# Kernel tuning notes

Hardware: AMD Instinct MI355X
Metric: run time of the kernel (lower is better)

## Reference

```python
import jax, jax.numpy as jnp
import numpy as np

N, DEG, C, D = 4096, 12, 4, 2
E = N * DEG
P = 2 * (D + 1) ** 2          # 18 radial MLPs: value set (s=0) + attention-key set (s=1)
R_MAX = (2 * D + 1) * C * C   # largest radial output size = 80


def _ln(x, g, b, eps=1e-5):
    mu = jnp.mean(x, axis=-1, keepdims=True)
    var = jnp.mean((x - mu) ** 2, axis=-1, keepdims=True)
    return (x - mu) / jnp.sqrt(var + eps) * g + b


def setup_inputs() -> dict:
    key = jax.random.key(0)
    ks = jax.random.split(key, 40)
    inp = {}
    inp["u"] = jax.random.randint(ks[0], (E,), 0, N)   # src nodes
    inp["v"] = jnp.repeat(jnp.arange(N), DEG)           # dst nodes: every node has DEG in-edges
    inp["dist"] = jax.random.uniform(ks[1], (E,))
    for k in range(D + 1):
        inp[f"f{k}"] = jax.random.normal(ks[2 + k], (N, C, 2 * k + 1))
    i = 5
    for k in range(D + 1):
        for l in range(D + 1):
            J = 2 * min(k, l) + 1
            inp[f"wj_{k}{l}"] = jax.random.normal(ks[i], (E, J, 2 * l + 1, 2 * k + 1)) * 0.2
            i += 1
    inp["wq"] = jax.random.normal(ks[i], (D + 1, C, C)) * 0.4; i += 1
    inp["rad_W1"] = jax.random.normal(ks[i], (P, 16, C + 1)) * 0.3; i += 1
    inp["rad_b1"] = jnp.zeros((P, 16)); inp["rad_g1"] = jnp.ones((P, 16)); inp["rad_be1"] = jnp.zeros((P, 16))
    inp["rad_W2"] = jax.random.normal(ks[i], (P, 16, 16)) * 0.25; i += 1
    inp["rad_b2"] = jnp.zeros((P, 16)); inp["rad_g2"] = jnp.ones((P, 16)); inp["rad_be2"] = jnp.zeros((P, 16))
    inp["rad_W3"] = jax.random.normal(ks[i], (P, R_MAX, 16)) * 0.2; i += 1
    inp["rad_b3"] = jnp.zeros((P, R_MAX))
    inp["si_W1"] = jax.random.normal(ks[i], (D + 1, C * C, C * C)) * 0.25; i += 1
    inp["si_b1"] = jnp.zeros((D + 1, C * C)); inp["si_g1"] = jnp.ones((D + 1, C * C)); inp["si_be1"] = jnp.zeros((D + 1, C * C))
    inp["si_W2"] = jax.random.normal(ks[i], (D + 1, C * C, C * C)) * 0.25; i += 1
    inp["si_b2"] = jnp.zeros((D + 1, C * C)); inp["si_g2"] = jnp.ones((D + 1, C * C)); inp["si_be2"] = jnp.zeros((D + 1, C * C))
    inp["si_W3"] = jax.random.normal(ks[i], (D + 1, C * C, C * C)) * 0.25; i += 1
    inp["si_b3"] = jnp.zeros((D + 1, C * C))
    return inp


def _forward(u, v, dist, f0, f1, f2,
             wj_00, wj_01, wj_02, wj_10, wj_11, wj_12, wj_20, wj_21, wj_22,
             wq, rad_W1, rad_b1, rad_g1, rad_be1, rad_W2, rad_b2, rad_g2, rad_be2, rad_W3, rad_b3,
             si_W1, si_b1, si_g1, si_be1, si_W2, si_b2, si_g2, si_be2, si_W3, si_b3):
    f = [f0, f1, f2]
    wj = {(0, 0): wj_00, (0, 1): wj_01, (0, 2): wj_02,
          (1, 0): wj_10, (1, 1): wj_11, (1, 2): wj_12,
          (2, 0): wj_20, (2, 1): wj_21, (2, 2): wj_22}
    n = f0.shape[0]
    # shared radial input: per-channel <f0_u, f0_v> plus edge distance -> [E, C+1]
    iv = jnp.concatenate([jnp.sum(f0[u] * f0[v], axis=2), dist[:, None]], axis=1)

    def radial(p, J):
        r_size = J * C * C
        h = jax.nn.relu(_ln(iv @ rad_W1[p].T + rad_b1[p], rad_g1[p], rad_be1[p]))
        h = jax.nn.relu(_ln(h @ rad_W2[p].T + rad_b2[p], rad_g2[p], rad_be2[p]))
        return h @ rad_W3[p, :r_size].T + rad_b3[p, :r_size]

    def make_w(k, l, s):
        # WLayer: radial MLP -> [E, J, c_out, c_in], contracted with CG basis w_j
        J = 2 * min(k, l) + 1
        p = s * (D + 1) ** 2 + k * (D + 1) + l
        Rm = radial(p, J).reshape(-1, J, C, C)
        return jnp.einsum('ejoi,ejlk->eoilk', Rm, wj[(k, l)])  # [E,o,i,2l+1,2k+1]

    # --- attention (AttnBlock) ---
    q = jnp.concatenate([jnp.einsum('oi,nik->nok', wq[k], f[k]) for k in range(D + 1)], axis=2)  # [N,C,9]
    k_edge = jnp.concatenate([
        sum(jnp.einsum('eoilk,eik->eol', make_w(k, l, 1), f[k][v]) for k in range(D + 1))
        for l in range(D + 1)], axis=2)  # [E,C,9] (keys use dst features, as in calc_k)
    dot = jnp.einsum('eol,eol->e', q[v], k_edge)
    m = jax.ops.segment_max(dot, v, num_segments=n)
    lse = m + jnp.log(jax.ops.segment_sum(jnp.exp(dot - m[v]), v, num_segments=n))
    a = jnp.exp(dot - lse[v])  # edge softmax over incoming edges of each dst node

    # --- attention-weighted tensor-product messages + scatter-sum (update_all) ---
    outs = []
    for l in range(D + 1):
        vl = sum(jnp.einsum('e,eoilk,eik->eol', a, make_w(k, l, 0), f[k][u]) for k in range(D + 1))
        outs.append(jax.ops.segment_sum(vl, v, num_segments=n))  # [N,C,2l+1]

    # --- self-interaction ---
    for l in range(D + 1):
        inner = jnp.einsum('ncl,ndl->ncd', f[l], f[l]).reshape(n, C * C)
        h = jax.nn.relu(_ln(inner @ si_W1[l].T + si_b1[l], si_g1[l], si_be1[l]))
        h = jax.nn.relu(_ln(h @ si_W2[l].T + si_b2[l], si_g2[l], si_be2[l]))
        siw = (h @ si_W3[l].T + si_b3[l]).reshape(n, C, C)
        outs[l] = outs[l] + jnp.einsum('noi,nil->nol', siw, f[l])

    # concat degree outputs f_out[0..2] along the m-axis -> [N, C, 1+3+5]
    return jnp.concatenate(outs, axis=2)


def reference(u, v, dist, f0, f1, f2,
              wj_00, wj_01, wj_02, wj_10, wj_11, wj_12, wj_20, wj_21, wj_22,
              wq, rad_W1, rad_b1, rad_g1, rad_be1, rad_W2, rad_b2, rad_g2, rad_be2, rad_W3, rad_b3,
              si_W1, si_b1, si_g1, si_be1, si_W2, si_b2, si_g2, si_be2, si_W3, si_b3):
    return _forward(u, v, dist, f0, f1, f2,
                    wj_00, wj_01, wj_02, wj_10, wj_11, wj_12, wj_20, wj_21, wj_22,
                    wq, rad_W1, rad_b1, rad_g1, rad_be1, rad_W2, rad_b2, rad_g2, rad_be2, rad_W3, rad_b3,
                    si_W1, si_b1, si_g1, si_be1, si_W2, si_b2, si_g2, si_be2, si_W3, si_b3)
```

## Files before the change

kernel.cpp:

```cpp
#include <hip/hip_runtime.h>
#include <hip/hip_bf16.h>

#define DEG 12

struct GP {
  const int* u;
  const void* dist;
  const void* f0; const void* f1; const void* f2;
  const void* wj[9];
  const void* wq;
  const void *rW1,*rb1,*rg1,*rbe1,*rW2,*rb2,*rg2,*rbe2,*rW3,*rb3;
  const void *sW1,*sb1,*sg1,*sbe1,*sW2,*sb2,*sg2,*sbe2,*sW3,*sb3;
  void* out;
  const float* wsf;
};

#define WS_W1   0
#define WS_W2   1440
#define WS_W3   6048
#define WS_SI1  29088
#define WS_SI2  29856
#define WS_SI3  30624
#define WS_G1   31392
#define WS_BE1  31680
#define WS_G2   31968
#define WS_BE2  32256
#define WS_B1   32544
#define WS_B2   32832
#define WS_B3   33120
#define WS_TOTAL 34560

struct alignas(16) Smem {
  float sRm[DEG][308];
  float sG[DEG][276];
  float sH2[DEG][148];
  float sF[13][36];
  float sIv[DEG][5];
  float sQ[36];
  float sDot[DEG];
  float sA[DEG];
  float sVl[DEG][36];
  float sSIin[48], sSIh[48], sSIh2[48], sSiw[48];
};

__device__ __forceinline__ float ldv(const __hip_bfloat16* p, int i){ return __bfloat162float(p[i]); }
__device__ __forceinline__ float ldv(const float* p, int i){ return p[i]; }

__device__ __forceinline__ void load16(const __hip_bfloat16* ptr, float* out){
  const uint4* q = reinterpret_cast<const uint4*>(ptr);
  uint4 a = q[0]; uint4 b = q[1];
  unsigned w[8] = {a.x,a.y,a.z,a.w,b.x,b.y,b.z,b.w};
  #pragma unroll
  for (int i=0;i<8;i++){
    out[2*i]   = __uint_as_float(w[i] << 16);
    out[2*i+1] = __uint_as_float(w[i] & 0xffff0000u);
  }
}
__device__ __forceinline__ void load16(const float* ptr, float* out){
  const float4* q = reinterpret_cast<const float4*>(ptr);
  #pragma unroll
  for (int i=0;i<4;i++){
    float4 a = q[i];
    out[4*i]=a.x; out[4*i+1]=a.y; out[4*i+2]=a.z; out[4*i+3]=a.w;
  }
}

__device__ __forceinline__ void st(__hip_bfloat16* p, int i, float v){ p[i] = __float2bfloat16(v); }
__device__ __forceinline__ void st(float* p, int i, float v){ p[i] = v; }

template<typename WT>
__device__ __forceinline__ void ln_relu16(float* h, const WT* g, const WT* be){
  float mu = 0.f;
  #pragma unroll
  for (int c=0;c<16;c++) mu += h[c];
  mu *= 0.0625f;
  float var = 0.f;
  #pragma unroll
  for (int c=0;c<16;c++){ float d=h[c]-mu; var += d*d; }
  var *= 0.0625f;
  float inv = rsqrtf(var + 1e-5f);
  #pragma unroll
  for (int c=0;c<16;c++){
    float y = (h[c]-mu)*inv*ldv(g,c) + ldv(be,c);
    h[c] = fmaxf(y, 0.f);
  }
}

template<typename WT>
struct WPtr {
  const WT *w1,*w2,*w3,*si1,*si2,*si3,*g1,*be1,*g2,*be2,*b1,*b2,*b3;
};

template<typename WT>
__device__ __forceinline__ void radial12(int S, const WPtr<WT>& W, int t, Smem& s){
  const int pk = t/12, e = t%12;
  const int pp = S*9 + pk;
  const float x0=s.sIv[e][0],x1=s.sIv[e][1],x2=s.sIv[e][2],x3=s.sIv[e][3],x4=s.sIv[e][4];
  float h[16];
  #pragma unroll
  for (int r=0;r<16;r++){
    const WT* row = W.w1 + (pp*16+r)*5;
    h[r] = ldv(W.b1,pp*16+r) + ldv(row,0)*x0 + ldv(row,1)*x1
         + ldv(row,2)*x2 + ldv(row,3)*x3 + ldv(row,4)*x4;
  }
  ln_relu16(h, W.g1+pp*16, W.be1+pp*16);
  float h2[16];
  #pragma unroll
  for (int r=0;r<16;r++){
    float wf[16]; load16(W.w2 + (pp*16+r)*16, wf);
    float acc = ldv(W.b2,pp*16+r);
    #pragma unroll
    for (int c=0;c<16;c++) acc += wf[c]*h[c];
    h2[r]=acc;
  }
  ln_relu16(h2, W.g2+pp*16, W.be2+pp*16);
  float4* dst = (float4*)&s.sH2[e][pk*16];
  #pragma unroll
  for (int i=0;i<4;i++) dst[i] = make_float4(h2[4*i],h2[4*i+1],h2[4*i+2],h2[4*i+3]);
}

template<typename WT>
__device__ __forceinline__ void radial3(int S, const WPtr<WT>& W, int t, Smem& s){
  const int rq = t/3, eq = t%3;
  const int rflat = rq*4;
  constexpr int RS[10]={0,16,32,48,64,112,160,176,224,304};
  int kp=0;
  #pragma unroll
  for (int k=1;k<9;k++) if (rflat >= RS[k]) kp = k;
  const int rl = rflat - RS[kp];
  const int pp = S*9 + kp;
  const int wbase = (pp*80 + rl)*16;
  float b[4];
  #pragma unroll
  for (int r=0;r<4;r++) b[r] = ldv(W.b3, pp*80+rl+r);
  #pragma unroll
  for (int half=0; half<2; ++half){
    const int e0 = eq*4 + half*2, e1 = e0+1;
    const float4* hp0 = (const float4*)&s.sH2[e0][kp*16];
    const float4* hp1 = (const float4*)&s.sH2[e1][kp*16];
    float4 ha[4], hb[4];
    #pragma unroll
    for (int i=0;i<4;i++){ ha[i]=hp0[i]; hb[i]=hp1[i]; }
    float a0[4], a1[4];
    #pragma unroll
    for (int r=0;r<4;r++){
      float wf[16]; load16(W.w3 + wbase + r*16, wf);
      float s0=0.f, s1=0.f;
      const float* h0 = (const float*)&ha[0];
      const float* h1 = (const float*)&hb[0];
      #pragma unroll
      for (int c=0;c<16;c++){ s0 += wf[c]*h0[c]; s1 += wf[c]*h1[c]; }
      a0[r]=b[r]+s0; a1[r]=b[r]+s1;
    }
    *(float4*)&s.sRm[e0][rflat] = make_float4(a0[0],a0[1],a0[2],a0[3]);
    *(float4*)&s.sRm[e1][rflat] = make_float4(a1[0],a1[1],a1[2],a1[3]);
  }
}

template<typename T>
__device__ __forceinline__ void stage_g(int S, const GP& p, int tt, int n12, Smem& s){
  constexpr int GOFF[9]={0,4,16,36,40,76,136,140,176};
  #pragma unroll
  for (int kp=0;kp<9;kp++){
    const int kk=kp/3, ll=kp%3;
    const int mn = kk<ll?kk:ll;
    const int J=2*mn+1, Lm=2*ll+1, Km=2*kk+1;
    const int koff = (kk==0)?0:((kk==1)?4:16);
    const int goff = GOFF[kp];
    const T* wjp = (const T*)p.wj[kp];
    const int nt = 12*J*Lm;
    for (int q=tt; q<nt; q+=128){
      int e = q/(J*Lm), jl = q%(J*Lm);
      int j = jl/Lm, lm = jl%Lm;
      const T* w = wjp + ((size_t)((n12+e)*J + j)*Lm + lm)*Km;
      const float* fv = S ? &s.sF[12][koff] : &s.sF[e][koff];
      float a0=0.f,a1=0.f,a2=0.f,a3=0.f;
      #pragma unroll
      for (int km=0;km<Km;km++){
        float wv = ldv(w,km);
        a0 += wv*fv[0*Km+km];
        a1 += wv*fv[1*Km+km];
        a2 += wv*fv[2*Km+km];
        a3 += wv*fv[3*Km+km];
      }
      float* gd = &s.sG[e][goff];
      gd[(j*4+0)*Lm+lm]=a0;
      gd[(j*4+1)*Lm+lm]=a1;
      gd[(j*4+2)*Lm+lm]=a2;
      gd[(j*4+3)*Lm+lm]=a3;
    }
  }
}

template<typename T, typename WT>
__device__ void gconv_run(const GP& p, Smem& s, const WPtr<WT>& W){
  const int n = blockIdx.x;
  const int t = threadIdx.x;
  const int n12 = n*DEG;
  const T* f0=(const T*)p.f0; const T* f1=(const T*)p.f1; const T* f2=(const T*)p.f2;
  constexpr int ROFF[9]={0,16,32,48,64,112,160,176,224};
  constexpr int GOFF[9]={0,4,16,36,40,76,136,140,176};

  for (int q0=t; q0<13*36; q0+=256){
    int node=q0/36, j=q0%36;
    int idn = (node<DEG)? p.u[n12+node] : n;
    float v;
    if (j<4)       v = ldv(f0, idn*4  + j);
    else if (j<16) v = ldv(f1, idn*12 + (j-4));
    else           v = ldv(f2, idn*20 + (j-16));
    s.sF[node][j] = v;
  }
  __syncthreads();

  if (t<48){ int e=t>>2, c=t&3; s.sIv[e][c] = s.sF[e][c]*s.sF[12][c]; }
  else if (t<60){ int e=t-48; s.sIv[e][4] = ldv((const T*)p.dist, n12+e); }
  else if (t>=64 && t<100){
    int t2=t-64, o=t2/9, mc=t2%9;
    int k = (mc<1)?0:((mc<4)?1:2);
    int m = mc - ((k==0)?0:((k==1)?1:4));
    int koff=(k==0)?0:((k==1)?4:16), Km=2*k+1;
    float acc=0.f;
    #pragma unroll
    for (int i=0;i<4;i++) acc += ldv((const T*)p.wq,(k*4+o)*4+i) * s.sF[12][koff+i*Km+m];
    s.sQ[t2]=acc;
  } else if (t>=128 && t<176){
    int t3=t-128, l=t3/16, rr=t3%16, o=rr>>2, i=rr&3;
    int koff=(l==0)?0:((l==1)?4:16), Lm=2*l+1;
    float acc=0.f;
    for (int m=0;m<Lm;m++) acc += s.sF[12][koff+o*Lm+m]*s.sF[12][koff+i*Lm+m];
    s.sSIin[t3]=acc;
  }
  __syncthreads();

  if (t<108)       radial12(1, W, t, s);
  else if (t>=128) stage_g<T>(1, p, t-128, n12, s);
  __syncthreads();

  if (t<228) radial3(1, W, t, s);
  __syncthreads();

  if (t<192){
    const int e=t>>4, o=(t>>2)&3, i=t&3;
    float d=0.f;
    #pragma unroll
    for (int kp=0;kp<9;kp++){
      const int kk=kp/3, ll=kp%3;
      const int mn=kk<ll?kk:ll;
      const int J=2*mn+1, Lm=2*ll+1;
      const int loff=(ll==0)?0:((ll==1)?1:4);
      #pragma unroll
      for (int j=0;j<J;j++){
        float rm = s.sRm[e][ROFF[kp]+j*16+o*4+i];
        #pragma unroll
        for (int lm=0;lm<Lm;lm++)
          d += rm * s.sG[e][GOFF[kp]+(j*4+i)*Lm+lm] * s.sQ[o*9+loff+lm];
      }
    }
    d += __shfl_xor(d,1);
    d += __shfl_xor(d,2);
    d += __shfl_xor(d,4);
    d += __shfl_xor(d,8);
    if ((t&15)==0) s.sDot[e]=d;
  } else if (t<240){
    int idx=t-192, l=idx/16, r=idx%16;
    float wf[16]; load16(W.si1 + (l*16+r)*16, wf);
    float acc = ldv((const T*)p.sb1,l*16+r);
    #pragma unroll
    for (int c=0;c<16;c++) acc += wf[c]*s.sSIin[l*16+c];
    s.sSIh[idx]=acc;
  }
  __syncthreads();

  if (t<108)       radial12(0, W, t, s);
  else if (t==127){
    float mx=-1e30f;
    #pragma unroll
    for (int e=0;e<12;e++) mx = fmaxf(mx, s.sDot[e]);
    float ex[12]; float se=0.f;
    #pragma unroll
    for (int e=0;e<12;e++){ ex[e]=__expf(s.sDot[e]-mx); se += ex[e]; }
    #pragma unroll
    for (int e=0;e<12;e++) s.sA[e] = ex[e]/se;
  }
  else if (t>=128) stage_g<T>(0, p, t-128, n12, s);
  __syncthreads();

  if (t<228) radial3(0, W, t, s);
  __syncthreads();

  if (t>=64){
    for (int q=t-64; q<432; q+=192){
      int l,e,o,lm;
      if (q<48){ l=0; e=q>>2; o=q&3; lm=0; }
      else if (q<192){ int r=q-48; l=1; e=r/12; int r2=r%12; o=r2/3; lm=r2%3; }
      else { int r=q-192; l=2; e=r/20; int r2=r%20; o=r2/5; lm=r2%5; }
      const int Lm=2*l+1, loff=(l==0)?0:((l==1)?1:4);
      float acc=0.f;
      for (int kk=0;kk<3;kk++){
        const int kp=kk*3+l;
        const int mn=kk<l?kk:l;
        const int J=2*mn+1;
        for (int j=0;j<J;j++)
          #pragma unroll
          for (int i=0;i<4;i++)
            acc += s.sRm[e][ROFF[kp]+j*16+o*4+i] * s.sG[e][GOFF[kp]+(j*4+i)*Lm+lm];
      }
      s.sVl[e][o*9+loff+lm]=acc;
    }
  } else if (t<48){
    int l=t/16, r=t%16;
    float mu=0.f;
    #pragma unroll
    for (int c=0;c<16;c++) mu += s.sSIh[l*16+c];
    mu *= 0.0625f;
    float var=0.f;
    #pragma unroll
    for (int c=0;c<16;c++){ float d=s.sSIh[l*16+c]-mu; var+=d*d; }
    var *= 0.0625f;
    float inv = rsqrtf(var+1e-5f);
    float wf[16]; load16(W.si2 + (l*16+r)*16, wf);
    float acc = ldv((const T*)p.sb2,l*16+r);
    #pragma unroll
    for (int c=0;c<16;c++){
      float y = (s.sSIh[l*16+c]-mu)*inv*ldv((const T*)p.sg1,l*16+c) + ldv((const T*)p.sbe1,l*16+c);
      acc += wf[c]*fmaxf(y,0.f);
    }
    s.sSIh2[t]=acc;
  }
  __syncthreads();

  if (t<48){
    int l=t/16, r=t%16;
    float mu=0.f;
    #pragma unroll
    for (int c=0;c<16;c++) mu += s.sSIh2[l*16+c];
    mu *= 0.0625f;
    float var=0.f;
    #pragma unroll
    for (int c=0;c<16;c++){ float d=s.sSIh2[l*16+c]-mu; var+=d*d; }
    var *= 0.0625f;
    float inv = rsqrtf(var+1e-5f);
    float wf[16]; load16(W.si3 + (l*16+r)*16, wf);
    float acc = ldv((const T*)p.sb3,l*16+r);
    #pragma unroll
    for (int c=0;c<16;c++){
      float y = (s.sSIh2[l*16+c]-mu)*inv*ldv((const T*)p.sg2,l*16+c) + ldv((const T*)p.sbe2,l*16+c);
      acc += wf[c]*fmaxf(y,0.f);
    }
    s.sSiw[t]=acc;
  }
  __syncthreads();

  if (t<36){
    int o=t/9, mc=t%9;
    int l = (mc<1)?0:((mc<4)?1:2);
    int m = mc - ((l==0)?0:((l==1)?1:4));
    int koff=(l==0)?0:((l==1)?4:16), Lm=2*l+1;
    float acc=0.f;
    #pragma unroll
    for (int e=0;e<12;e++) acc += s.sA[e]*s.sVl[e][t];
    #pragma unroll
    for (int i=0;i<4;i++) acc += s.sSiw[l*16+o*4+i]*s.sF[12][koff+i*Lm+m];
    st((T*)p.out, n*36+t, acc);
  }
}

template<typename T>
__device__ __forceinline__ void gconv_dispatch(const GP& p, Smem& s){
  if (p.wsf){
    const float* w = p.wsf;
    WPtr<float> W{w+WS_W1, w+WS_W2, w+WS_W3, w+WS_SI1, w+WS_SI2, w+WS_SI3,
                  w+WS_G1, w+WS_BE1, w+WS_G2, w+WS_BE2, w+WS_B1, w+WS_B2, w+WS_B3};
    gconv_run<T,float>(p, s, W);
  } else {
    WPtr<T> W{(const T*)p.rW1,(const T*)p.rW2,(const T*)p.rW3,
              (const T*)p.sW1,(const T*)p.sW2,(const T*)p.sW3,
              (const T*)p.rg1,(const T*)p.rbe1,(const T*)p.rg2,(const T*)p.rbe2,
              (const T*)p.rb1,(const T*)p.rb2,(const T*)p.rb3};
    gconv_run<T,T>(p, s, W);
  }
}

__global__ __launch_bounds__(256,4) void gconv_kernel(GP p){
  __shared__ Smem s;
  const unsigned magic = *(const unsigned*)p.rg1;
  if (magic == 0x3F803F80u) gconv_dispatch<__hip_bfloat16>(p, s);
  else                      gconv_dispatch<float>(p, s);
}

template<typename T>
__device__ __forceinline__ void prep_body(const GP& p, float* ws, int i){
  float v;
  if      (i<WS_W2)  v = ldv((const T*)p.rW1,  i-WS_W1);
  else if (i<WS_W3)  v = ldv((const T*)p.rW2,  i-WS_W2);
  else if (i<WS_SI1) v = ldv((const T*)p.rW3,  i-WS_W3);
  else if (i<WS_SI2) v = ldv((const T*)p.sW1,  i-WS_SI1);
  else if (i<WS_SI3) v = ldv((const T*)p.sW2,  i-WS_SI2);
  else if (i<WS_G1)  v = ldv((const T*)p.sW3,  i-WS_SI3);
  else if (i<WS_BE1) v = ldv((const T*)p.rg1,  i-WS_G1);
  else if (i<WS_G2)  v = ldv((const T*)p.rbe1, i-WS_BE1);
  else if (i<WS_BE2) v = ldv((const T*)p.rg2,  i-WS_G2);
  else if (i<WS_B1)  v = ldv((const T*)p.rbe2, i-WS_BE2);
  else if (i<WS_B2)  v = ldv((const T*)p.rb1,  i-WS_B1);
  else if (i<WS_B3)  v = ldv((const T*)p.rb2,  i-WS_B2);
  else               v = ldv((const T*)p.rb3,  i-WS_B3);
  ws[i] = v;
}

__global__ void prep_kernel(GP p, float* ws){
  int i = blockIdx.x*256 + threadIdx.x;
  if (i >= WS_TOTAL) return;
  const unsigned magic = *(const unsigned*)p.rg1;
  if (magic == 0x3F803F80u) prep_body<__hip_bfloat16>(p, ws, i);
  else                      prep_body<float>(p, ws, i);
}

extern "C" void kernel_launch(void* const* d_in, const int* in_sizes, int n_in,
                              void* d_out, int out_size, void* d_ws, size_t ws_size,
                              hipStream_t stream) {
  GP p;
  p.u    = (const int*)d_in[0];
  p.dist = d_in[2];
  p.f0   = d_in[3];
  p.f1   = d_in[4];
  p.f2   = d_in[5];
  for (int kp=0;kp<9;kp++) p.wj[kp] = d_in[6+kp];
  p.wq   = d_in[15];
  p.rW1  = d_in[16]; p.rb1  = d_in[17]; p.rg1  = d_in[18]; p.rbe1 = d_in[19];
  p.rW2  = d_in[20]; p.rb2  = d_in[21]; p.rg2  = d_in[22]; p.rbe2 = d_in[23];
  p.rW3  = d_in[24]; p.rb3  = d_in[25];
  p.sW1  = d_in[26]; p.sb1  = d_in[27]; p.sg1  = d_in[28]; p.sbe1 = d_in[29];
  p.sW2  = d_in[30]; p.sb2  = d_in[31]; p.sg2  = d_in[32]; p.sbe2 = d_in[33];
  p.sW3  = d_in[34]; p.sb3  = d_in[35];
  p.out  = d_out;

  const bool use_ws = (ws_size >= (size_t)WS_TOTAL*sizeof(float));
  p.wsf = use_ws ? (const float*)d_ws : nullptr;

  if (use_ws)
    prep_kernel<<<dim3((WS_TOTAL+255)/256), dim3(256), 0, stream>>>(p, (float*)d_ws);
  gconv_kernel<<<dim3(4096), dim3(256), 0, stream>>>(p);
}
```

Baseline: 269.7 us.

## Fold radial output contraction into radial3 and drop sRm shared buffer

The last radial layer now contracts its outputs directly with the staged G tensor, accumulating attention dot products and value vectors into shared memory with atomics. This removes the 12x308 sRm buffer and two separate contraction phases with their barriers. The self-interaction MLP steps are moved onto otherwise idle threads of earlier phases. Launch bounds rise to 6 blocks per SM to take advantage of the smaller shared footprint. The cost is shared-memory atomic contention and register pressure under the tighter bound.

```diff
diff --git a/kernel.cpp b/kernel.cpp
--- a/kernel.cpp
+++ b/kernel.cpp
@@ -31,15 +31,14 @@
 #define WS_TOTAL 34560
 
 struct alignas(16) Smem {
-  float sRm[DEG][308];
   float sG[DEG][276];
   float sH2[DEG][148];
   float sF[13][36];
+  float sVl[DEG][36];
   float sIv[DEG][5];
   float sQ[36];
   float sDot[DEG];
   float sA[DEG];
-  float sVl[DEG][36];
   float sSIin[48], sSIh[48], sSIh2[48], sSiw[48];
 };
 
@@ -119,26 +118,33 @@
   for (int i=0;i<4;i++) dst[i] = make_float4(h2[4*i],h2[4*i+1],h2[4*i+2],h2[4*i+3]);
 }
 
-template<typename WT>
-__device__ __forceinline__ void radial3(int S, const WPtr<WT>& W, int t, Smem& s){
+template<int S, typename WT>
+__device__ __forceinline__ void radial3fold(const WPtr<WT>& W, int t, Smem& s){
+  constexpr int GOFF[9]={0,4,16,36,40,76,136,140,176};
+  constexpr int RS[10]={0,16,32,48,64,112,160,176,224,304};
   const int rq = t/3, eq = t%3;
   const int rflat = rq*4;
-  constexpr int RS[10]={0,16,32,48,64,112,160,176,224,304};
   int kp=0;
   #pragma unroll
   for (int k=1;k<9;k++) if (rflat >= RS[k]) kp = k;
   const int rl = rflat - RS[kp];
+  const int j = rl>>4, o=(rl>>2)&3;
   const int pp = S*9 + kp;
   const int wbase = (pp*80 + rl)*16;
+  const int ll = kp%3;
+  const int Lm = 2*ll+1;
+  const int loff = (ll==0)?0:((ll==1)?1:4);
+  const int goff = GOFF[kp] + (j*4)*Lm;
   float b[4];
   #pragma unroll
   for (int r=0;r<4;r++) b[r] = ldv(W.b3, pp*80+rl+r);
+
   #pragma unroll
   for (int half=0; half<2; ++half){
     const int e0 = eq*4 + half*2, e1 = e0+1;
+    float4 ha[4], hb[4];
     const float4* hp0 = (const float4*)&s.sH2[e0][kp*16];
     const float4* hp1 = (const float4*)&s.sH2[e1][kp*16];
-    float4 ha[4], hb[4];
     #pragma unroll
     for (int i=0;i<4;i++){ ha[i]=hp0[i]; hb[i]=hp1[i]; }
     float a0[4], a1[4];
@@ -146,14 +152,31 @@
     for (int r=0;r<4;r++){
       float wf[16]; load16(W.w3 + wbase + r*16, wf);
       float s0=0.f, s1=0.f;
-      const float* h0 = (const float*)&ha[0];
-      const float* h1 = (const float*)&hb[0];
+      const float* h0=(const float*)ha; const float* h1=(const float*)hb;
       #pragma unroll
       for (int c=0;c<16;c++){ s0 += wf[c]*h0[c]; s1 += wf[c]*h1[c]; }
       a0[r]=b[r]+s0; a1[r]=b[r]+s1;
     }
-    *(float4*)&s.sRm[e0][rflat] = make_float4(a0[0],a0[1],a0[2],a0[3]);
-    *(float4*)&s.sRm[e1][rflat] = make_float4(a1[0],a1[1],a1[2],a1[3]);
+    const float* g0 = &s.sG[e0][goff];
+    const float* g1 = &s.sG[e1][goff];
+    if (S==1){
+      float d0=0.f, d1=0.f;
+      for (int lm=0; lm<Lm; lm++){
+        float q = s.sQ[o*9+loff+lm];
+        float u0 = a0[0]*g0[lm] + a0[1]*g0[Lm+lm] + a0[2]*g0[2*Lm+lm] + a0[3]*g0[3*Lm+lm];
+        float u1 = a1[0]*g1[lm] + a1[1]*g1[Lm+lm] + a1[2]*g1[2*Lm+lm] + a1[3]*g1[3*Lm+lm];
+        d0 += q*u0; d1 += q*u1;
+      }
+      atomicAdd(&s.sDot[e0], d0);
+      atomicAdd(&s.sDot[e1], d1);
+    } else {
+      for (int lm=0; lm<Lm; lm++){
+        float u0 = a0[0]*g0[lm] + a0[1]*g0[Lm+lm] + a0[2]*g0[2*Lm+lm] + a0[3]*g0[3*Lm+lm];
+        float u1 = a1[0]*g1[lm] + a1[1]*g1[Lm+lm] + a1[2]*g1[2*Lm+lm] + a1[3]*g1[3*Lm+lm];
+        atomicAdd(&s.sVl[e0][o*9+loff+lm], u0);
+        atomicAdd(&s.sVl[e1][o*9+loff+lm], u1);
+      }
+    }
   }
 }
 
@@ -198,8 +221,6 @@
   const int t = threadIdx.x;
   const int n12 = n*DEG;
   const T* f0=(const T*)p.f0; const T* f1=(const T*)p.f1; const T* f2=(const T*)p.f2;
-  constexpr int ROFF[9]={0,16,32,48,64,112,160,176,224};
-  constexpr int GOFF[9]={0,4,16,36,40,76,136,140,176};
 
   for (int q0=t; q0<13*36; q0+=256){
     int node=q0/36, j=q0%36;
@@ -210,6 +231,11 @@
     else           v = ldv(f2, idn*20 + (j-16));
     s.sF[node][j] = v;
   }
+  {
+    float* z = &s.sVl[0][0];
+    for (int q=t; q<432; q+=256) z[q]=0.f;
+    if (t<12) s.sDot[t]=0.f;
+  }
   __syncthreads();
 
   if (t<48){ int e=t>>2, c=t&3; s.sIv[e][c] = s.sF[e][c]*s.sF[12][c]; }
@@ -232,46 +258,25 @@
   }
   __syncthreads();
 
-  if (t<108)       radial12(1, W, t, s);
-  else if (t>=128) stage_g<T>(1, p, t-128, n12, s);
-  __syncthreads();
-
-  if (t<228) radial3(1, W, t, s);
-  __syncthreads();
-
-  if (t<192){
-    const int e=t>>4, o=(t>>2)&3, i=t&3;
-    float d=0.f;
-    #pragma unroll
-    for (int kp=0;kp<9;kp++){
-      const int kk=kp/3, ll=kp%3;
-      const int mn=kk<ll?kk:ll;
-      const int J=2*mn+1, Lm=2*ll+1;
-      const int loff=(ll==0)?0:((ll==1)?1:4);
-      #pragma unroll
-      for (int j=0;j<J;j++){
-        float rm = s.sRm[e][ROFF[kp]+j*16+o*4+i];
-        #pragma unroll
-        for (int lm=0;lm<Lm;lm++)
-          d += rm * s.sG[e][GOFF[kp]+(j*4+i)*Lm+lm] * s.sQ[o*9+loff+lm];
-      }
-    }
-    d += __shfl_xor(d,1);
-    d += __shfl_xor(d,2);
-    d += __shfl_xor(d,4);
-    d += __shfl_xor(d,8);
-    if ((t&15)==0) s.sDot[e]=d;
-  } else if (t<240){
-    int idx=t-192, l=idx/16, r=idx%16;
-    float wf[16]; load16(W.si1 + (l*16+r)*16, wf);
-    float acc = ldv((const T*)p.sb1,l*16+r);
-    #pragma unroll
-    for (int c=0;c<16;c++) acc += wf[c]*s.sSIin[l*16+c];
-    s.sSIh[idx]=acc;
-  }
-  __syncthreads();
-
-  if (t<108)       radial12(0, W, t, s);
+  if (t<108) radial12(1, W, t, s);
+  else if (t>=128){
+    stage_g<T>(1, p, t-128, n12, s);
+    const int tt=t-128;
+    if (tt<48){
+      int l=tt/16, r=tt%16;
+      float wf[16]; load16(W.si1 + (l*16+r)*16, wf);
+      float acc = ldv((const T*)p.sb1,l*16+r);
+      #pragma unroll
+      for (int c=0;c<16;c++) acc += wf[c]*s.sSIin[l*16+c];
+      s.sSIh[tt]=acc;
+    }
+  }
+  __syncthreads();
+
+  if (t<228) radial3fold<1>(W, t, s);
+  __syncthreads();
+
+  if (t<108) radial12(0, W, t, s);
   else if (t==127){
     float mx=-1e30f;
     #pragma unroll
@@ -282,72 +287,54 @@
     #pragma unroll
     for (int e=0;e<12;e++) s.sA[e] = ex[e]/se;
   }
-  else if (t>=128) stage_g<T>(0, p, t-128, n12, s);
-  __syncthreads();
-
-  if (t<228) radial3(0, W, t, s);
-  __syncthreads();
-
-  if (t>=64){
-    for (int q=t-64; q<432; q+=192){
-      int l,e,o,lm;
-      if (q<48){ l=0; e=q>>2; o=q&3; lm=0; }
-      else if (q<192){ int r=q-48; l=1; e=r/12; int r2=r%12; o=r2/3; lm=r2%3; }
-      else { int r=q-192; l=2; e=r/20; int r2=r%20; o=r2/5; lm=r2%5; }
-      const int Lm=2*l+1, loff=(l==0)?0:((l==1)?1:4);
-      float acc=0.f;
-      for (int kk=0;kk<3;kk++){
-        const int kp=kk*3+l;
-        const int mn=kk<l?kk:l;
-        const int J=2*mn+1;
-        for (int j=0;j<J;j++)
-          #pragma unroll
-          for (int i=0;i<4;i++)
-            acc += s.sRm[e][ROFF[kp]+j*16+o*4+i] * s.sG[e][GOFF[kp]+(j*4+i)*Lm+lm];
+  else if (t>=128){
+    stage_g<T>(0, p, t-128, n12, s);
+    const int tt=t-128;
+    if (tt<48){
+      int l=tt/16, r=tt%16;
+      float mu=0.f;
+      #pragma unroll
+      for (int c=0;c<16;c++) mu += s.sSIh[l*16+c];
+      mu *= 0.0625f;
+      float var=0.f;
+      #pragma unroll
+      for (int c=0;c<16;c++){ float d=s.sSIh[l*16+c]-mu; var+=d*d; }
+      var *= 0.0625f;
+      float inv = rsqrtf(var+1e-5f);
+      float wf[16]; load16(W.si2 + (l*16+r)*16, wf);
+      float acc = ldv((const T*)p.sb2,l*16+r);
+      #pragma unroll
+      for (int c=0;c<16;c++){
+        float y = (s.sSIh[l*16+c]-mu)*inv*ldv((const T*)p.sg1,l*16+c) + ldv((const T*)p.sbe1,l*16+c);
+        acc += wf[c]*fmaxf(y,0.f);
       }
-      s.sVl[e][o*9+loff+lm]=acc;
-    }
-  } else if (t<48){
-    int l=t/16, r=t%16;
-    float mu=0.f;
-    #pragma unroll
-    for (int c=0;c<16;c++) mu += s.sSIh[l*16+c];
-    mu *= 0.0625f;
-    float var=0.f;
-    #pragma unroll
-    for (int c=0;c<16;c++){ float d=s.sSIh[l*16+c]-mu; var+=d*d; }
-    var *= 0.0625f;
-    float inv = rsqrtf(var+1e-5f);
-    float wf[16]; load16(W.si2 + (l*16+r)*16, wf);
-    float acc = ldv((const T*)p.sb2,l*16+r);
-    #pragma unroll
-    for (int c=0;c<16;c++){
-      float y = (s.sSIh[l*16+c]-mu)*inv*ldv((const T*)p.sg1,l*16+c) + ldv((const T*)p.sbe1,l*16+c);
-      acc += wf[c]*fmaxf(y,0.f);
-    }
-    s.sSIh2[t]=acc;
-  }
-  __syncthreads();
-
-  if (t<48){
-    int l=t/16, r=t%16;
-    float mu=0.f;
-    #pragma unroll
-    for (int c=0;c<16;c++) mu += s.sSIh2[l*16+c];
-    mu *= 0.0625f;
-    float var=0.f;
-    #pragma unroll
-    for (int c=0;c<16;c++){ float d=s.sSIh2[l*16+c]-mu; var+=d*d; }
-    var *= 0.0625f;
-    float inv = rsqrtf(var+1e-5f);
-    float wf[16]; load16(W.si3 + (l*16+r)*16, wf);
-    float acc = ldv((const T*)p.sb3,l*16+r);
-    #pragma unroll
-    for (int c=0;c<16;c++){
-      float y = (s.sSIh2[l*16+c]-mu)*inv*ldv((const T*)p.sg2,l*16+c) + ldv((const T*)p.sbe2,l*16+c);
-      acc += wf[c]*fmaxf(y,0.f);
-    }
-    s.sSiw[t]=acc;
+      s.sSIh2[tt]=acc;
+    }
+  }
+  __syncthreads();
+
+  if (t<228) radial3fold<0>(W, t, s);
+  else {
+    for (int q=t-228; q<48; q+=28){
+      int l=q/16, r=q%16;
+      float mu=0.f;
+      #pragma unroll
+      for (int c=0;c<16;c++) mu += s.sSIh2[l*16+c];
+      mu *= 0.0625f;
+      float var=0.f;
+      #pragma unroll
+      for (int c=0;c<16;c++){ float d=s.sSIh2[l*16+c]-mu; var+=d*d; }
+      var *= 0.0625f;
+      float inv = rsqrtf(var+1e-5f);
+      float wf[16]; load16(W.si3 + (l*16+r)*16, wf);
+      float acc = ldv((const T*)p.sb3,l*16+r);
+      #pragma unroll
+      for (int c=0;c<16;c++){
+        float y = (s.sSIh2[l*16+c]-mu)*inv*ldv((const T*)p.sg2,l*16+c) + ldv((const T*)p.sbe2,l*16+c);
+        acc += wf[c]*fmaxf(y,0.f);
+      }
+      s.sSiw[q]=acc;
+    }
   }
   __syncthreads();
 
@@ -381,7 +368,7 @@
   }
 }
 
-__global__ __launch_bounds__(256,4) void gconv_kernel(GP p){
+__global__ __launch_bounds__(256,6) void gconv_kernel(GP p){
   __shared__ Smem s;
   const unsigned magic = *(const unsigned*)p.rg1;
   if (magic == 0x3F803F80u) gconv_dispatch<__hip_bfloat16>(p, s);
```

After: 572.5 us. +112.2%, slower.

## Split radial MLP rows across thread pairs and rebalance per-stage thread work

Applied to the files above, without the earlier changes.

Each radial-MLP (pp,edge) unit is now handled by two threads, each computing 8 of the 16 hidden rows, with layer-norm statistics and activations exchanged via shuffles, so 216 threads work instead of 108. Stage assignments are reshuffled: the self-interaction MLP layers move into the idle lanes of the radial stages, stage_g for the value set runs on all 256 threads in its own phase, and the value contraction uses all threads. This aims to shorten the serial critical path of each block's barrier-separated phases, at the cost of extra shuffles and duplicate weight-row loads per pair, plus one added barrier phase.

```diff
diff --git a/kernel.cpp b/kernel.cpp
--- a/kernel.cpp
+++ b/kernel.cpp
@@ -69,54 +69,75 @@
 __device__ __forceinline__ void st(float* p, int i, float v){ p[i] = v; }
 
 template<typename WT>
-__device__ __forceinline__ void ln_relu16(float* h, const WT* g, const WT* be){
-  float mu = 0.f;
-  #pragma unroll
-  for (int c=0;c<16;c++) mu += h[c];
-  mu *= 0.0625f;
-  float var = 0.f;
-  #pragma unroll
-  for (int c=0;c<16;c++){ float d=h[c]-mu; var += d*d; }
-  var *= 0.0625f;
-  float inv = rsqrtf(var + 1e-5f);
-  #pragma unroll
-  for (int c=0;c<16;c++){
-    float y = (h[c]-mu)*inv*ldv(g,c) + ldv(be,c);
-    h[c] = fmaxf(y, 0.f);
-  }
-}
-
-template<typename WT>
 struct WPtr {
   const WT *w1,*w2,*w3,*si1,*si2,*si3,*g1,*be1,*g2,*be2,*b1,*b2,*b3;
 };
 
 template<typename WT>
-__device__ __forceinline__ void radial12(int S, const WPtr<WT>& W, int t, Smem& s){
-  const int pk = t/12, e = t%12;
+__device__ __forceinline__ void radial12_split(int S, const WPtr<WT>& W, int t, Smem& s){
+  const int u = t>>1, b = t&1;
+  const int pk = u/12, e = u%12;
   const int pp = S*9 + pk;
+  const int rbase = pp*16 + b*8;
   const float x0=s.sIv[e][0],x1=s.sIv[e][1],x2=s.sIv[e][2],x3=s.sIv[e][3],x4=s.sIv[e][4];
-  float h[16];
-  #pragma unroll
-  for (int r=0;r<16;r++){
-    const WT* row = W.w1 + (pp*16+r)*5;
-    h[r] = ldv(W.b1,pp*16+r) + ldv(row,0)*x0 + ldv(row,1)*x1
+  float h[8];
+  #pragma unroll
+  for (int r=0;r<8;r++){
+    const WT* row = W.w1 + (rbase+r)*5;
+    h[r] = ldv(W.b1,rbase+r) + ldv(row,0)*x0 + ldv(row,1)*x1
          + ldv(row,2)*x2 + ldv(row,3)*x3 + ldv(row,4)*x4;
   }
-  ln_relu16(h, W.g1+pp*16, W.be1+pp*16);
-  float h2[16];
-  #pragma unroll
-  for (int r=0;r<16;r++){
-    float wf[16]; load16(W.w2 + (pp*16+r)*16, wf);
-    float acc = ldv(W.b2,pp*16+r);
-    #pragma unroll
-    for (int c=0;c<16;c++) acc += wf[c]*h[c];
+  float s1=0.f;
+  #pragma unroll
+  for (int c=0;c<8;c++) s1 += h[c];
+  s1 += __shfl_xor(s1,1);
+  const float mu = s1*0.0625f;
+  float v1=0.f;
+  #pragma unroll
+  for (int c=0;c<8;c++){ float d=h[c]-mu; v1 += d*d; }
+  v1 += __shfl_xor(v1,1);
+  const float inv = rsqrtf(v1*0.0625f + 1e-5f);
+  #pragma unroll
+  for (int c=0;c<8;c++){
+    float y = (h[c]-mu)*inv*ldv(W.g1,rbase+c) + ldv(W.be1,rbase+c);
+    h[c] = fmaxf(y,0.f);
+  }
+  float lo[8], hi[8];
+  #pragma unroll
+  for (int c=0;c<8;c++){
+    float o = __shfl_xor(h[c],1);
+    lo[c] = b ? o : h[c];
+    hi[c] = b ? h[c] : o;
+  }
+  float h2[8];
+  #pragma unroll
+  for (int r=0;r<8;r++){
+    float wf[16]; load16(W.w2 + (rbase+r)*16, wf);
+    float acc = ldv(W.b2,rbase+r);
+    #pragma unroll
+    for (int c=0;c<8;c++) acc += wf[c]*lo[c];
+    #pragma unroll
+    for (int c=0;c<8;c++) acc += wf[8+c]*hi[c];
     h2[r]=acc;
   }
-  ln_relu16(h2, W.g2+pp*16, W.be2+pp*16);
-  float4* dst = (float4*)&s.sH2[e][pk*16];
-  #pragma unroll
-  for (int i=0;i<4;i++) dst[i] = make_float4(h2[4*i],h2[4*i+1],h2[4*i+2],h2[4*i+3]);
+  float s2=0.f;
+  #pragma unroll
+  for (int c=0;c<8;c++) s2 += h2[c];
+  s2 += __shfl_xor(s2,1);
+  const float mu2 = s2*0.0625f;
+  float v2=0.f;
+  #pragma unroll
+  for (int c=0;c<8;c++){ float d=h2[c]-mu2; v2 += d*d; }
+  v2 += __shfl_xor(v2,1);
+  const float inv2 = rsqrtf(v2*0.0625f + 1e-5f);
+  #pragma unroll
+  for (int c=0;c<8;c++){
+    float y = (h2[c]-mu2)*inv2*ldv(W.g2,rbase+c) + ldv(W.be2,rbase+c);
+    h2[c] = fmaxf(y,0.f);
+  }
+  float4* dst = (float4*)&s.sH2[e][pk*16 + b*8];
+  dst[0] = make_float4(h2[0],h2[1],h2[2],h2[3]);
+  dst[1] = make_float4(h2[4],h2[5],h2[6],h2[7]);
 }
 
 template<typename WT>
@@ -158,7 +179,7 @@
 }
 
 template<typename T>
-__device__ __forceinline__ void stage_g(int S, const GP& p, int tt, int n12, Smem& s){
+__device__ __forceinline__ void stage_g(int S, const GP& p, int tt, int nthr, int n12, Smem& s){
   constexpr int GOFF[9]={0,4,16,36,40,76,136,140,176};
   #pragma unroll
   for (int kp=0;kp<9;kp++){
@@ -169,7 +190,7 @@
     const int goff = GOFF[kp];
     const T* wjp = (const T*)p.wj[kp];
     const int nt = 12*J*Lm;
-    for (int q=tt; q<nt; q+=128){
+    for (int q=tt; q<nt; q+=nthr){
       int e = q/(J*Lm), jl = q%(J*Lm);
       int j = jl/Lm, lm = jl%Lm;
       const T* w = wjp + ((size_t)((n12+e)*J + j)*Lm + lm)*Km;
@@ -223,17 +244,28 @@
     #pragma unroll
     for (int i=0;i<4;i++) acc += ldv((const T*)p.wq,(k*4+o)*4+i) * s.sF[12][koff+i*Km+m];
     s.sQ[t2]=acc;
-  } else if (t>=128 && t<176){
-    int t3=t-128, l=t3/16, rr=t3%16, o=rr>>2, i=rr&3;
+  } else if (t>=100 && t<148){
+    int t3=t-100, l=t3/16, rr=t3%16, o=rr>>2, i=rr&3;
     int koff=(l==0)?0:((l==1)?4:16), Lm=2*l+1;
     float acc=0.f;
     for (int m=0;m<Lm;m++) acc += s.sF[12][koff+o*Lm+m]*s.sF[12][koff+i*Lm+m];
     s.sSIin[t3]=acc;
-  }
-  __syncthreads();
-
-  if (t<108)       radial12(1, W, t, s);
-  else if (t>=128) stage_g<T>(1, p, t-128, n12, s);
+  } else if (t>=148){
+    stage_g<T>(1, p, t-148, 108, n12, s);
+  }
+  __syncthreads();
+
+  if (t<216) radial12_split(1, W, t, s);
+  else {
+    for (int q=t-216; q<48; q+=40){
+      int l=q/16, r=q%16;
+      float wf[16]; load16(W.si1 + (l*16+r)*16, wf);
+      float acc = ldv((const T*)p.sb1,l*16+r);
+      #pragma unroll
+      for (int c=0;c<16;c++) acc += wf[c]*s.sSIin[l*16+c];
+      s.sSIh[q]=acc;
+    }
+  }
   __syncthreads();
 
   if (t<228) radial3(1, W, t, s);
@@ -263,52 +295,6 @@
     if ((t&15)==0) s.sDot[e]=d;
   } else if (t<240){
     int idx=t-192, l=idx/16, r=idx%16;
-    float wf[16]; load16(W.si1 + (l*16+r)*16, wf);
-    float acc = ldv((const T*)p.sb1,l*16+r);
-    #pragma unroll
-    for (int c=0;c<16;c++) acc += wf[c]*s.sSIin[l*16+c];
-    s.sSIh[idx]=acc;
-  }
-  __syncthreads();
-
-  if (t<108)       radial12(0, W, t, s);
-  else if (t==127){
-    float mx=-1e30f;
-    #pragma unroll
-    for (int e=0;e<12;e++) mx = fmaxf(mx, s.sDot[e]);
-    float ex[12]; float se=0.f;
-    #pragma unroll
-    for (int e=0;e<12;e++){ ex[e]=__expf(s.sDot[e]-mx); se += ex[e]; }
-    #pragma unroll
-    for (int e=0;e<12;e++) s.sA[e] = ex[e]/se;
-  }
-  else if (t>=128) stage_g<T>(0, p, t-128, n12, s);
-  __syncthreads();
-
-  if (t<228) radial3(0, W, t, s);
-  __syncthreads();
-
-  if (t>=64){
-    for (int q=t-64; q<432; q+=192){
-      int l,e,o,lm;
-      if (q<48){ l=0; e=q>>2; o=q&3; lm=0; }
-      else if (q<192){ int r=q-48; l=1; e=r/12; int r2=r%12; o=r2/3; lm=r2%3; }
-      else { int r=q-192; l=2; e=r/20; int r2=r%20; o=r2/5; lm=r2%5; }
-      const int Lm=2*l+1, loff=(l==0)?0:((l==1)?1:4);
-      float acc=0.f;
-      for (int kk=0;kk<3;kk++){
-        const int kp=kk*3+l;
-        const int mn=kk<l?kk:l;
-        const int J=2*mn+1;
-        for (int j=0;j<J;j++)
-          #pragma unroll
-          for (int i=0;i<4;i++)
-            acc += s.sRm[e][ROFF[kp]+j*16+o*4+i] * s.sG[e][GOFF[kp]+(j*4+i)*Lm+lm];
-      }
-      s.sVl[e][o*9+loff+lm]=acc;
-    }
-  } else if (t<48){
-    int l=t/16, r=t%16;
     float mu=0.f;
     #pragma unroll
     for (int c=0;c<16;c++) mu += s.sSIh[l*16+c];
@@ -325,29 +311,68 @@
       float y = (s.sSIh[l*16+c]-mu)*inv*ldv((const T*)p.sg1,l*16+c) + ldv((const T*)p.sbe1,l*16+c);
       acc += wf[c]*fmaxf(y,0.f);
     }
-    s.sSIh2[t]=acc;
-  }
-  __syncthreads();
-
-  if (t<48){
-    int l=t/16, r=t%16;
-    float mu=0.f;
-    #pragma unroll
-    for (int c=0;c<16;c++) mu += s.sSIh2[l*16+c];
-    mu *= 0.0625f;
-    float var=0.f;
-    #pragma unroll
-    for (int c=0;c<16;c++){ float d=s.sSIh2[l*16+c]-mu; var+=d*d; }
-    var *= 0.0625f;
-    float inv = rsqrtf(var+1e-5f);
-    float wf[16]; load16(W.si3 + (l*16+r)*16, wf);
-    float acc = ldv((const T*)p.sb3,l*16+r);
-    #pragma unroll
-    for (int c=0;c<16;c++){
-      float y = (s.sSIh2[l*16+c]-mu)*inv*ldv((const T*)p.sg2,l*16+c) + ldv((const T*)p.sbe2,l*16+c);
-      acc += wf[c]*fmaxf(y,0.f);
-    }
-    s.sSiw[t]=acc;
+    s.sSIh2[idx]=acc;
+  }
+  __syncthreads();
+
+  stage_g<T>(0, p, t, 256, n12, s);
+  __syncthreads();
+
+  if (t<216) radial12_split(0, W, t, s);
+  else {
+    for (int q=t-216; q<48; q+=40){
+      int l=q/16, r=q%16;
+      float mu=0.f;
+      #pragma unroll
+      for (int c=0;c<16;c++) mu += s.sSIh2[l*16+c];
+      mu *= 0.0625f;
+      float var=0.f;
+      #pragma unroll
+      for (int c=0;c<16;c++){ float d=s.sSIh2[l*16+c]-mu; var+=d*d; }
+      var *= 0.0625f;
+      float inv = rsqrtf(var+1e-5f);
+      float wf[16]; load16(W.si3 + (l*16+r)*16, wf);
+      float acc = ldv((const T*)p.sb3,l*16+r);
+      #pragma unroll
+      for (int c=0;c<16;c++){
+        float y = (s.sSIh2[l*16+c]-mu)*inv*ldv((const T*)p.sg2,l*16+c) + ldv((const T*)p.sbe2,l*16+c);
+        acc += wf[c]*fmaxf(y,0.f);
+      }
+      s.sSiw[q]=acc;
+    }
+  }
+  __syncthreads();
+
+  if (t<228) radial3(0, W, t, s);
+  else if (t==240){
+    float mx=-1e30f;
+    #pragma unroll
+    for (int e=0;e<12;e++) mx = fmaxf(mx, s.sDot[e]);
+    float ex[12]; float se=0.f;
+    #pragma unroll
+    for (int e=0;e<12;e++){ ex[e]=__expf(s.sDot[e]-mx); se += ex[e]; }
+    #pragma unroll
+    for (int e=0;e<12;e++) s.sA[e] = ex[e]/se;
+  }
+  __syncthreads();
+
+  for (int q=t; q<432; q+=256){
+    int l,e,o,lm;
+    if (q<48){ l=0; e=q>>2; o=q&3; lm=0; }
+    else if (q<192){ int r=q-48; l=1; e=r/12; int r2=r%12; o=r2/3; lm=r2%3; }
+    else { int r=q-192; l=2; e=r/20; int r2=r%20; o=r2/5; lm=r2%5; }
+    const int Lm=2*l+1, loff=(l==0)?0:((l==1)?1:4);
+    float acc=0.f;
+    for (int kk=0;kk<3;kk++){
+      const int kp=kk*3+l;
+      const int mn=kk<l?kk:l;
+      const int J=2*mn+1;
+      for (int j=0;j<J;j++)
+        #pragma unroll
+        for (int i=0;i<4;i++)
+          acc += s.sRm[e][ROFF[kp]+j*16+o*4+i] * s.sG[e][GOFF[kp]+(j*4+i)*Lm+lm];
+    }
+    s.sVl[e][o*9+loff+lm]=acc;
   }
   __syncthreads();
 
```

Measured after the change: 310.7 us. 15.2% more time.

## Compute radial MLP output layer with bf16 MFMA instead of scalar FMAs

Applied to the files above, without the earlier changes.

Replaces the scalar third radial-MLP layer (16→up-to-80 outputs per edge) with 16x16x32 bf16 MFMA tiles. A new prep kernel repacks W3 into the MFMA A-operand layout in workspace, and radial12 writes the hidden activations as bf16 into a union buffer in B-operand layout. The 32-wide K dimension is half-padded with zeros, duplicating data. This cuts per-thread FMA and global weight loads, at the cost of bf16 rounding of weights and activations and wasted MFMA work.

```diff
diff --git a/kernel.cpp b/kernel.cpp
--- a/kernel.cpp
+++ b/kernel.cpp
@@ -2,6 +2,9 @@
 #include <hip/hip_bf16.h>
 
 #define DEG 12
+
+typedef short short8v __attribute__((ext_vector_type(8)));
+typedef float float4v __attribute__((ext_vector_type(4)));
 
 struct GP {
   const int* u;
@@ -13,6 +16,7 @@
   const void *sW1,*sb1,*sg1,*sbe1,*sW2,*sb2,*sg2,*sbe2,*sW3,*sb3;
   void* out;
   const float* wsf;
+  const unsigned short* wA;
 };
 
 #define WS_W1   0
@@ -29,11 +33,15 @@
 #define WS_B2   32832
 #define WS_B3   33120
 #define WS_TOTAL 34560
+#define WS_A_HALF 19456
 
 struct alignas(16) Smem {
   float sRm[DEG][308];
   float sG[DEG][276];
-  float sH2[DEG][148];
+  union {
+    float sH2[DEG][148];
+    unsigned short sB[9][4][16][4];
+  };
   float sF[13][36];
   float sIv[DEG][5];
   float sQ[36];
@@ -68,6 +76,11 @@
 __device__ __forceinline__ void st(__hip_bfloat16* p, int i, float v){ p[i] = __float2bfloat16(v); }
 __device__ __forceinline__ void st(float* p, int i, float v){ p[i] = v; }
 
+__device__ __forceinline__ unsigned short f2bf(float v){
+  __hip_bfloat16 b = __float2bfloat16(v);
+  return *reinterpret_cast<unsigned short*>(&b);
+}
+
 template<typename WT>
 __device__ __forceinline__ void ln_relu16(float* h, const WT* g, const WT* be){
   float mu = 0.f;
@@ -92,7 +105,7 @@
 };
 
 template<typename WT>
-__device__ __forceinline__ void radial12(int S, const WPtr<WT>& W, int t, Smem& s){
+__device__ __forceinline__ void radial12(int S, const WPtr<WT>& W, int t, Smem& s, bool mf){
   const int pk = t/12, e = t%12;
   const int pp = S*9 + pk;
   const float x0=s.sIv[e][0],x1=s.sIv[e][1],x2=s.sIv[e][2],x3=s.sIv[e][3],x4=s.sIv[e][4];
@@ -114,9 +127,14 @@
     h2[r]=acc;
   }
   ln_relu16(h2, W.g2+pp*16, W.be2+pp*16);
-  float4* dst = (float4*)&s.sH2[e][pk*16];
-  #pragma unroll
-  for (int i=0;i<4;i++) dst[i] = make_float4(h2[4*i],h2[4*i+1],h2[4*i+2],h2[4*i+3]);
+  if (mf){
+    #pragma unroll
+    for (int c=0;c<16;c++) s.sB[pk][c>>2][e][c&3] = f2bf(h2[c]);
+  } else {
+    float4* dst = (float4*)&s.sH2[e][pk*16];
+    #pragma unroll
+    for (int i=0;i<4;i++) dst[i] = make_float4(h2[4*i],h2[4*i+1],h2[4*i+2],h2[4*i+3]);
+  }
 }
 
 template<typename WT>
@@ -154,6 +172,44 @@
     }
     *(float4*)&s.sRm[e0][rflat] = make_float4(a0[0],a0[1],a0[2],a0[3]);
     *(float4*)&s.sRm[e1][rflat] = make_float4(a1[0],a1[1],a1[2],a1[3]);
+  }
+}
+
+__device__ __forceinline__ void radial3_mfma(int S, const float* wsf,
+                                             const unsigned short* wA, int t, Smem& s){
+  const int wave = t>>6, lane = t&63;
+  const int col = lane&15, kq = lane>>4;
+  #pragma unroll
+  for (int t5=0; t5<5; ++t5){
+    const int tile = wave + t5*4;
+    if (tile < 19){
+      const int rflat = tile*16;
+      int kp=0;
+      if (rflat>=16)  kp=1;
+      if (rflat>=32)  kp=2;
+      if (rflat>=48)  kp=3;
+      if (rflat>=64)  kp=4;
+      if (rflat>=112) kp=5;
+      if (rflat>=160) kp=6;
+      if (rflat>=176) kp=7;
+      if (rflat>=224) kp=8;
+      const int rs = (kp==0)?0:(kp==1)?16:(kp==2)?32:(kp==3)?48:(kp==4)?64:(kp==5)?112:(kp==6)?160:(kp==7)?176:224;
+      const int rl = rflat - rs;
+      const int pp = S*9 + kp;
+      short8v a = *reinterpret_cast<const short8v*>(wA + (size_t)(S*19+tile)*512 + (size_t)lane*8);
+      const unsigned short* bp = &s.sB[kp][kq][col][0];
+      short4 blo = *reinterpret_cast<const short4*>(bp);
+      short8v b;
+      b[0]=blo.x; b[1]=blo.y; b[2]=blo.z; b[3]=blo.w;
+      b[4]=blo.x; b[5]=blo.y; b[6]=blo.z; b[7]=blo.w;
+      float4v c; c[0]=0.f; c[1]=0.f; c[2]=0.f; c[3]=0.f;
+      float4v d = __builtin_amdgcn_mfma_f32_16x16x32_bf16(a, b, c, 0, 0, 0);
+      if (col < 12){
+        const float4 bb = *reinterpret_cast<const float4*>(wsf + WS_B3 + pp*80 + rl + kq*4);
+        *(float4*)&s.sRm[col][rflat + kq*4] =
+          make_float4(d[0]+bb.x, d[1]+bb.y, d[2]+bb.z, d[3]+bb.w);
+      }
+    }
   }
 }
 
@@ -193,7 +249,7 @@
 }
 
 template<typename T, typename WT>
-__device__ void gconv_run(const GP& p, Smem& s, const WPtr<WT>& W){
+__device__ void gconv_run(const GP& p, Smem& s, const WPtr<WT>& W, bool mf){
   const int n = blockIdx.x;
   const int t = threadIdx.x;
   const int n12 = n*DEG;
@@ -232,11 +288,12 @@
   }
   __syncthreads();
 
-  if (t<108)       radial12(1, W, t, s);
+  if (t<108)       radial12(1, W, t, s, mf);
   else if (t>=128) stage_g<T>(1, p, t-128, n12, s);
   __syncthreads();
 
-  if (t<228) radial3(1, W, t, s);
+  if (mf)          radial3_mfma(1, p.wsf, p.wA, t, s);
+  else if (t<228)  radial3(1, W, t, s);
   __syncthreads();
 
   if (t<192){
@@ -271,7 +328,7 @@
   }
   __syncthreads();
 
-  if (t<108)       radial12(0, W, t, s);
+  if (t<108)       radial12(0, W, t, s, mf);
   else if (t==127){
     float mx=-1e30f;
     #pragma unroll
@@ -285,7 +342,8 @@
   else if (t>=128) stage_g<T>(0, p, t-128, n12, s);
   __syncthreads();
 
-  if (t<228) radial3(0, W, t, s);
+  if (mf)          radial3_mfma(0, p.wsf, p.wA, t, s);
+  else if (t<228)  radial3(0, W, t, s);
   __syncthreads();
 
   if (t>=64){
@@ -371,13 +429,13 @@
     const float* w = p.wsf;
     WPtr<float> W{w+WS_W1, w+WS_W2, w+WS_W3, w+WS_SI1, w+WS_SI2, w+WS_SI3,
                   w+WS_G1, w+WS_BE1, w+WS_G2, w+WS_BE2, w+WS_B1, w+WS_B2, w+WS_B3};
-    gconv_run<T,float>(p, s, W);
+    gconv_run<T,float>(p, s, W, p.wA != nullptr);
   } else {
     WPtr<T> W{(const T*)p.rW1,(const T*)p.rW2,(const T*)p.rW3,
               (const T*)p.sW1,(const T*)p.sW2,(const T*)p.sW3,
               (const T*)p.rg1,(const T*)p.rbe1,(const T*)p.rg2,(const T*)p.rbe2,
               (const T*)p.rb1,(const T*)p.rb2,(const T*)p.rb3};
-    gconv_run<T,T>(p, s, W);
+    gconv_run<T,T>(p, s, W, false);
   }
 }
 
@@ -413,6 +471,38 @@
   const unsigned magic = *(const unsigned*)p.rg1;
   if (magic == 0x3F803F80u) prep_body<__hip_bfloat16>(p, ws, i);
   else                      prep_body<float>(p, ws, i);
+}
+
+__global__ void prep2_kernel(GP p, unsigned short* wsA){
+  int i = blockIdx.x*256 + threadIdx.x;
+  if (i >= 2*19*512) return;
+  const unsigned magic = *(const unsigned*)p.rg1;
+  int st   = i>>9;
+  int lane = (i>>3)&63;
+  int j    = i&7;
+  int S = st/19, tile = st%19;
+  int rflat = tile*16;
+  int kp=0;
+  if (rflat>=16)  kp=1;
+  if (rflat>=32)  kp=2;
+  if (rflat>=48)  kp=3;
+  if (rflat>=64)  kp=4;
+  if (rflat>=112) kp=5;
+  if (rflat>=160) kp=6;
+  if (rflat>=176) kp=7;
+  if (rflat>=224) kp=8;
+  const int rs = (kp==0)?0:(kp==1)?16:(kp==2)?32:(kp==3)?48:(kp==4)?64:(kp==5)?112:(kp==6)?160:(kp==7)?176:224;
+  const int rl = rflat - rs;
+  const int pp = S*9 + kp;
+  const int row = lane&15;
+  const int k = 4*(lane>>4) + (j&3);
+  float v = 0.f;
+  if (j < 4){
+    int idx = (pp*80 + rl + row)*16 + k;
+    v = (magic==0x3F803F80u) ? ldv((const __hip_bfloat16*)p.rW3, idx)
+                             : ldv((const float*)p.rW3, idx);
+  }
+  wsA[i] = f2bf(v);
 }
 
 extern "C" void kernel_launch(void* const* d_in, const int* in_sizes, int n_in,
@@ -435,9 +525,14 @@
   p.out  = d_out;
 
   const bool use_ws = (ws_size >= (size_t)WS_TOTAL*sizeof(float));
+  const bool use_mf = (ws_size >= (size_t)WS_TOTAL*sizeof(float) + (size_t)WS_A_HALF*sizeof(unsigned short));
   p.wsf = use_ws ? (const float*)d_ws : nullptr;
+  unsigned short* wsA = use_mf ? (unsigned short*)((float*)d_ws + WS_TOTAL) : nullptr;
+  p.wA = wsA;
 
   if (use_ws)
     prep_kernel<<<dim3((WS_TOTAL+255)/256), dim3(256), 0, stream>>>(p, (float*)d_ws);
+  if (use_mf)
+    prep2_kernel<<<dim3((2*19*512+255)/256), dim3(256), 0, stream>>>(p, wsA);
   gconv_kernel<<<dim3(4096), dim3(256), 0, stream>>>(p);
 }
```

Result: faster. 258.5 us (-4.2%).
